# Optimization experiments

Hardware: AMD Instinct MI355X
Metric: run time of the kernel (lower is better)

The kernel has to match this reference:

```python
import jax, jax.numpy as jnp
import numpy as np

ROUTING_ITERS = 3
EPS = 1e-12


def squash(s):
    # squash over both pose-matrix dims (axis=[-2,-1])
    n2 = jnp.sum(s * s, axis=(-2, -1), keepdims=True)
    n = jnp.sqrt(n2 + EPS)
    return s * (n2 / (1.0 + n2)) / n


def setup_inputs() -> dict:
    key = jax.random.key(0)
    k1, k2, k3 = jax.random.split(key, 3)
    B, I, O = 32, 4096, 32
    input_poses = jax.random.normal(k1, (B, I, 4, 4), dtype=jnp.float32)
    input_activations = jax.random.uniform(k2, (B, I), dtype=jnp.float32)
    # weight: [num_capsules, num_input_caps, 4, 4] (trans_in=trans_out=False for 4x4->4x4)
    w = jax.random.normal(k3, (O, I, 4, 4), dtype=jnp.float32) * 0.05
    return {"input_poses": input_poses, "input_activations": input_activations, "w": w}


def reference(input_poses, input_activations, w):
    # votes: expand_dims(poses,1) @ w, broadcast over output capsules -> [B,O,I,4,4]
    votes = jnp.einsum("bixy,oiyz->boixz", input_poses, w)
    B, O, I = votes.shape[0], votes.shape[1], votes.shape[2]

    # dynamic routing (routing-by-agreement)
    b = jnp.zeros((B, O, I), dtype=votes.dtype)
    s = None
    for it in range(ROUTING_ITERS):
        c = jax.nn.softmax(b, axis=1)  # couple over output capsules
        s = jnp.einsum("boi,boixy->boxy", c, votes)  # weighted sum [B,O,4,4]
        if it < ROUTING_ITERS - 1:
            v = squash(s)
            b = b + jnp.einsum("boixy,boxy->boi", votes, v)

    capsule_poses = squash(s)  # activation == 'squash'
    capsule_activations = jnp.sqrt(jnp.sum(capsule_poses * capsule_poses, axis=(-2, -1)) + EPS)
    return capsule_poses, capsule_activations
```

## Files before the change

kernel.cpp:

```cpp
#include <hip/hip_runtime.h>
#include <math.h>


#define NB 32
#define NI 4096
#define NO 32
#define I_TILE 16
#define NCHUNK (NI / I_TILE)
#define B_TILE 8
#define NBG (NB / B_TILE)
#define SOFF (NB * NO * 16)
#define EPSF 1e-12f

#define W_OSTR 10
#define W_ISTR (32 * W_OSTR)
#define W_WORDS (I_TILE * W_ISTR)
#define P_WORDS (B_TILE * I_TILE * 8)

typedef _Float16 v2h __attribute__((ext_vector_type(2)));

#if __has_builtin(__builtin_amdgcn_fdot2)
__device__ __forceinline__ float fdot2(v2h a, v2h b, float c) {
    return __builtin_amdgcn_fdot2(a, b, c, false);
}
#else
__device__ __forceinline__ float fdot2(v2h a, v2h b, float c) {
    return fmaf((float)a.x, (float)b.x, fmaf((float)a.y, (float)b.y, c));
}
#endif

#if __has_builtin(__builtin_amdgcn_cvt_pkrtz)
__device__ __forceinline__ v2h pk2h(float a, float b) {
    return __builtin_bit_cast(v2h, __builtin_amdgcn_cvt_pkrtz(a, b));
}
#else
__device__ __forceinline__ v2h pk2h(float a, float b) {
    v2h r; r.x = (_Float16)a; r.y = (_Float16)b; return r;
}
#endif

__device__ __forceinline__ v2h bch(unsigned u) {
    return __builtin_bit_cast(v2h, u);
}

__device__ __forceinline__ float dot4(const float4 a, const float4 b) {
    return fmaf(a.x, b.x, fmaf(a.y, b.y, fmaf(a.z, b.z, a.w * b.w)));
}

__device__ __forceinline__ void fma4(float4& s, const float c, const float4 t) {
    s.x = fmaf(c, t.x, s.x);
    s.y = fmaf(c, t.y, s.y);
    s.z = fmaf(c, t.z, s.z);
    s.w = fmaf(c, t.w, s.w);
}

template <int CTRL>
__device__ __forceinline__ float dpp_add(float x) {
    int xi = __builtin_bit_cast(int, x);
    int yi = __builtin_amdgcn_update_dpp(0, xi, CTRL, 0xf, 0xf, false);
    return x + __builtin_bit_cast(float, yi);
}

__device__ __forceinline__ float sum32(float x) {
    x = dpp_add<0xB1>(x);
    x = dpp_add<0x4E>(x);
    x = dpp_add<0x141>(x);
    x = dpp_add<0x140>(x);
#if __has_builtin(__builtin_amdgcn_permlane16_swap)
    typedef unsigned uv2 __attribute__((ext_vector_type(2)));
    const unsigned xi = __builtin_bit_cast(unsigned, x);
    uv2 r = __builtin_amdgcn_permlane16_swap(xi, xi, false, false);
    return __builtin_bit_cast(float, r.x) + __builtin_bit_cast(float, r.y);
#else
    int t = __builtin_amdgcn_ds_swizzle(__builtin_bit_cast(int, x), 0x401F);
    return x + __builtin_bit_cast(float, t);
#endif
}

__global__ __launch_bounds__(256, 4) void caps_pass_h(
    const float* __restrict__ poses, const float* __restrict__ w,
    const float* __restrict__ v_buf, float* __restrict__ s_part,
    const int pass)
{
    __shared__ unsigned wsw[W_WORDS];
    __shared__ unsigned psw[P_WORDS];
    const int tid    = threadIdx.x;
    const int chunk  = blockIdx.x;
    const int bgroup = blockIdx.y;
    const int ibase  = chunk * I_TILE;

    #pragma unroll
    for (int r = 0; r < 4; ++r) {
        const int idx = r * 256 + tid;
        const int o_l = idx >> 5;
        const int l   = idx & 31;
        const int i_l = l >> 1;
        const int m   = l & 1;
        const float* g = w + (((size_t)o_l * NI + ibase + i_l) << 4) + (m << 3);
        const float4 A = *(const float4*)g;
        const float4 B = *(const float4*)(g + 4);
        const v2h c0 = pk2h(A.x, B.x), c1 = pk2h(A.y, B.y);
        const v2h c2 = pk2h(A.z, B.z), c3 = pk2h(A.w, B.w);
        const int base = i_l * W_ISTR + o_l * W_OSTR + (m << 2);
        *(uint2*)&wsw[base]     = make_uint2(__builtin_bit_cast(unsigned, c0),
                                             __builtin_bit_cast(unsigned, c1));
        *(uint2*)&wsw[base + 2] = make_uint2(__builtin_bit_cast(unsigned, c2),
                                             __builtin_bit_cast(unsigned, c3));
    }
    #pragma unroll
    for (int r = 0; r < 2; ++r) {
        const int idx = r * 256 + tid;
        const int b_l = idx >> 6;
        const int l   = idx & 63;
        const int i_l = l >> 2;
        const int x   = l & 3;
        const float4 row = *(const float4*)(
            poses + (((size_t)(bgroup * B_TILE + b_l) * NI + ibase + i_l) << 4)
                  + (x << 2));
        const v2h c0 = pk2h(row.x, row.y), c1 = pk2h(row.z, row.w);
        *(uint2*)&psw[((b_l * I_TILE + i_l) << 3) + (x << 1)] =
            make_uint2(__builtin_bit_cast(unsigned, c0),
                       __builtin_bit_cast(unsigned, c1));
    }

    const int o    = tid & 31;
    const int bsub = tid >> 5;
    const int b    = bgroup * B_TILE + bsub;
    const int bo   = b * NO + o;

    float4 vv0 = {0,0,0,0}, vv1 = {0,0,0,0}, vv2 = {0,0,0,0}, vv3 = {0,0,0,0};
    if (pass > 0) {
        const float4* vp = (const float4*)(v_buf + (bo << 4));
        vv0 = vp[0]; vv1 = vp[1]; vv2 = vp[2]; vv3 = vp[3];
    }

    const unsigned* wrow = &wsw[o * W_OSTR];
    const unsigned* prow = &psw[(bsub * I_TILE) << 3];

    __syncthreads();

    float4 s0 = {0,0,0,0}, s1 = {0,0,0,0}, s2 = {0,0,0,0}, s3 = {0,0,0,0};

    #pragma unroll 2
    for (int i = 0; i < I_TILE; ++i) {
        const uint2 wa = *(const uint2*)&wrow[i * W_ISTR + 0];
        const uint2 wb = *(const uint2*)&wrow[i * W_ISTR + 2];
        const uint2 wc = *(const uint2*)&wrow[i * W_ISTR + 4];
        const uint2 wd = *(const uint2*)&wrow[i * W_ISTR + 6];
        const uint4 pa = *(const uint4*)&prow[(i << 3) + 0];
        const uint4 pb = *(const uint4*)&prow[(i << 3) + 4];

        const v2h p00 = bch(pa.x), p01 = bch(pa.y);
        const v2h p10 = bch(pa.z), p11 = bch(pa.w);
        const v2h p20 = bch(pb.x), p21 = bch(pb.y);
        const v2h p30 = bch(pb.z), p31 = bch(pb.w);
        const v2h w00 = bch(wa.x), w01 = bch(wa.y);
        const v2h w02 = bch(wb.x), w03 = bch(wb.y);
        const v2h w10 = bch(wc.x), w11 = bch(wc.y);
        const v2h w12 = bch(wd.x), w13 = bch(wd.y);

        float4 t0, t1, t2, t3;
        t0.x = fdot2(p00, w00, fdot2(p01, w10, 0.0f));
        t0.y = fdot2(p00, w01, fdot2(p01, w11, 0.0f));
        t0.z = fdot2(p00, w02, fdot2(p01, w12, 0.0f));
        t0.w = fdot2(p00, w03, fdot2(p01, w13, 0.0f));
        t1.x = fdot2(p10, w00, fdot2(p11, w10, 0.0f));
        t1.y = fdot2(p10, w01, fdot2(p11, w11, 0.0f));
        t1.z = fdot2(p10, w02, fdot2(p11, w12, 0.0f));
        t1.w = fdot2(p10, w03, fdot2(p11, w13, 0.0f));
        t2.x = fdot2(p20, w00, fdot2(p21, w10, 0.0f));
        t2.y = fdot2(p20, w01, fdot2(p21, w11, 0.0f));
        t2.z = fdot2(p20, w02, fdot2(p21, w12, 0.0f));
        t2.w = fdot2(p20, w03, fdot2(p21, w13, 0.0f));
        t3.x = fdot2(p30, w00, fdot2(p31, w10, 0.0f));
        t3.y = fdot2(p30, w01, fdot2(p31, w11, 0.0f));
        t3.z = fdot2(p30, w02, fdot2(p31, w12, 0.0f));
        t3.w = fdot2(p30, w03, fdot2(p31, w13, 0.0f));

        float cc;
        if (pass == 0) {
            cc = 1.0f / 32.0f;
        } else {
            const float d = dot4(t0,vv0) + dot4(t1,vv1)
                          + dot4(t2,vv2) + dot4(t3,vv3);
            const float e  = __expf(d);
            const float es = sum32(e);
            cc = __fdividef(e, es);
        }
        fma4(s0, cc, t0); fma4(s1, cc, t1);
        fma4(s2, cc, t2); fma4(s3, cc, t3);
    }

    float4* sp = (float4*)(s_part + ((size_t)chunk * (NB * NO) + bo) * 16);
    sp[0] = s0; sp[1] = s1; sp[2] = s2; sp[3] = s3;
}

__global__ __launch_bounds__(256) void caps_reduce(
    const float* __restrict__ s_part, float* __restrict__ v_buf,
    float* __restrict__ out, const int pass)
{
    const int e  = threadIdx.x & 63;
    const int c4 = threadIdx.x >> 6;
    const int eg = blockIdx.x * 64 + e;

    float acc = 0.0f;
    #pragma unroll 8
    for (int j = 0; j < NCHUNK / 4; ++j) {
        const int c = c4 * (NCHUNK / 4) + j;
        acc += s_part[(size_t)c * SOFF + eg];
    }
    __shared__ float red[4][64];
    red[c4][e] = acc;
    __syncthreads();

    if (threadIdx.x < 64) {
        const float a = red[0][e] + red[1][e] + red[2][e] + red[3][e];
        float x = a * a;
        #pragma unroll
        for (int msk = 8; msk >= 1; msk >>= 1)
            x += __shfl_xor(x, msk, 16);
        const float n2 = x;
        const float n  = sqrtf(n2 + EPSF);
        const float sc = (n2 / (1.0f + n2)) / n;
        if (pass < 2) {
            const float vold = (pass == 0) ? 0.0f : v_buf[eg];
            v_buf[eg] = fmaf(sc, a, vold);
        } else {
            out[eg] = sc * a;
            if ((e & 15) == 0)
                out[NB * NO * 16 + (eg >> 4)] = sqrtf(n2 * sc * sc + EPSF);
        }
    }
}

#define FB_CHUNKS 32
#define FB_IPB (NI / FB_CHUNKS)

__device__ __forceinline__ float4 row_mm(const float4 p, const float4 w0,
                                         const float4 w1, const float4 w2,
                                         const float4 w3) {
    float4 r;
    r.x = fmaf(p.x, w0.x, fmaf(p.y, w1.x, fmaf(p.z, w2.x, p.w * w3.x)));
    r.y = fmaf(p.x, w0.y, fmaf(p.y, w1.y, fmaf(p.z, w2.y, p.w * w3.y)));
    r.z = fmaf(p.x, w0.z, fmaf(p.y, w1.z, fmaf(p.z, w2.z, p.w * w3.z)));
    r.w = fmaf(p.x, w0.w, fmaf(p.y, w1.w, fmaf(p.z, w2.w, p.w * w3.w)));
    return r;
}

__global__ __launch_bounds__(256) void caps_pass_fb(
    const float* __restrict__ poses, const float* __restrict__ w,
    const float* __restrict__ v_buf, float* __restrict__ s_buf, const int mode)
{
    const int tid   = threadIdx.x;
    const int b     = blockIdx.y;
    const int chunk = blockIdx.x;
    const int o     = tid & 31;
    const int g     = tid >> 5;

    float4 v0 = {0,0,0,0}, v1 = {0,0,0,0}, v2 = {0,0,0,0}, v3 = {0,0,0,0};
    if (mode != 0) {
        const float4* vp = (const float4*)(v_buf + (((b * NO) + o) << 4));
        v0 = vp[0]; v1 = vp[1]; v2 = vp[2]; v3 = vp[3];
    }
    float4 s0 = {0,0,0,0}, s1 = {0,0,0,0}, s2 = {0,0,0,0}, s3 = {0,0,0,0};
    const int ibase = chunk * FB_IPB + g;
    #pragma unroll 4
    for (int it = 0; it < FB_IPB / 8; ++it) {
        const int i = ibase + (it << 3);
        const float4* ppf = (const float4*)(poses + ((((size_t)b * NI) + i) << 4));
        const float4 p0 = ppf[0], p1 = ppf[1], p2 = ppf[2], p3 = ppf[3];
        const float4* wpf = (const float4*)(w + ((((size_t)o * NI) + i) << 4));
        const float4 w0 = wpf[0], w1 = wpf[1], w2 = wpf[2], w3 = wpf[3];
        const float4 t0 = row_mm(p0, w0, w1, w2, w3);
        const float4 t1 = row_mm(p1, w0, w1, w2, w3);
        const float4 t2 = row_mm(p2, w0, w1, w2, w3);
        const float4 t3 = row_mm(p3, w0, w1, w2, w3);
        float cc;
        if (mode == 0) {
            cc = 1.0f / 32.0f;
        } else {
            float d = dot4(t0,v0) + dot4(t1,v1) + dot4(t2,v2) + dot4(t3,v3);
            const float e  = __expf(d);
            const float es = sum32(e);
            cc = __fdividef(e, es);
        }
        fma4(s0, cc, t0); fma4(s1, cc, t1);
        fma4(s2, cc, t2); fma4(s3, cc, t3);
    }
    __shared__ float red[8][32][16];
    float4* rp = (float4*)&red[g][o][0];
    rp[0] = s0; rp[1] = s1; rp[2] = s2; rp[3] = s3;
    __syncthreads();
    for (int idx = tid; idx < NO * 16; idx += 256) {
        const int oo = idx >> 4;
        const int k  = idx & 15;
        float acc = red[0][oo][k];
        #pragma unroll
        for (int gg = 1; gg < 8; ++gg) acc += red[gg][oo][k];
        atomicAdd(&s_buf[(((b * NO) + oo) << 4) + k], acc);
    }
}

__global__ __launch_bounds__(256) void caps_squash_fb(
    float* __restrict__ s_buf, float* __restrict__ v_buf,
    float* __restrict__ out, const int mode)
{
    const int idx = blockIdx.x * 256 + threadIdx.x;
    if (idx >= NB * NO) return;
    float4* sp = (float4*)(s_buf + (idx << 4));
    const float4 s0 = sp[0], s1 = sp[1], s2 = sp[2], s3 = sp[3];
    const float n2 = dot4(s0,s0) + dot4(s1,s1) + dot4(s2,s2) + dot4(s3,s3);
    const float n  = sqrtf(n2 + EPSF);
    const float sc = (n2 / (1.0f + n2)) / n;
    if (mode == 2) {
        float4* op = (float4*)(out + (idx << 4));
        op[0] = make_float4(sc*s0.x, sc*s0.y, sc*s0.z, sc*s0.w);
        op[1] = make_float4(sc*s1.x, sc*s1.y, sc*s1.z, sc*s1.w);
        op[2] = make_float4(sc*s2.x, sc*s2.y, sc*s2.z, sc*s2.w);
        op[3] = make_float4(sc*s3.x, sc*s3.y, sc*s3.z, sc*s3.w);
        out[NB * NO * 16 + idx] = sqrtf(n2 * sc * sc + EPSF);
    } else {
        float4* vp = (float4*)(v_buf + (idx << 4));
        float4 a0 = {0,0,0,0}, a1 = {0,0,0,0}, a2 = {0,0,0,0}, a3 = {0,0,0,0};
        if (mode != 0) { a0 = vp[0]; a1 = vp[1]; a2 = vp[2]; a3 = vp[3]; }
        vp[0] = make_float4(fmaf(sc,s0.x,a0.x), fmaf(sc,s0.y,a0.y), fmaf(sc,s0.z,a0.z), fmaf(sc,s0.w,a0.w));
        vp[1] = make_float4(fmaf(sc,s1.x,a1.x), fmaf(sc,s1.y,a1.y), fmaf(sc,s1.z,a1.z), fmaf(sc,s1.w,a1.w));
        vp[2] = make_float4(fmaf(sc,s2.x,a2.x), fmaf(sc,s2.y,a2.y), fmaf(sc,s2.z,a2.z), fmaf(sc,s2.w,a2.w));
        vp[3] = make_float4(fmaf(sc,s3.x,a3.x), fmaf(sc,s3.y,a3.y), fmaf(sc,s3.z,a3.z), fmaf(sc,s3.w,a3.w));
        const float4 z = {0,0,0,0};
        sp[0] = z; sp[1] = z; sp[2] = z; sp[3] = z;
    }
}

extern "C" void kernel_launch(void* const* d_in, const int* in_sizes, int n_in,
                              void* d_out, int out_size, void* d_ws, size_t ws_size,
                              hipStream_t stream) {
    const float* poses = (const float*)d_in[0];
    const float* w     = (const float*)d_in[2];
    float* out = (float*)d_out;

    const size_t need = ((size_t)NCHUNK * SOFF + SOFF) * sizeof(float);
    if (ws_size >= need) {
        float* s_part = (float*)d_ws;
        float* v_buf  = s_part + (size_t)NCHUNK * SOFF;
        dim3 gp(NCHUNK, NBG), blk(256), gr(256);
        for (int pass = 0; pass < 3; ++pass) {
            caps_pass_h<<<gp, blk, 0, stream>>>(poses, w, v_buf, s_part, pass);
            caps_reduce<<<gr, blk, 0, stream>>>(s_part, v_buf, out, pass);
        }
    } else {
        float* s_buf = (float*)d_ws;
        float* v_buf = s_buf + SOFF;
        (void)hipMemsetAsync(s_buf, 0, SOFF * sizeof(float), stream);
        dim3 grid(FB_CHUNKS, NB), block(256);
        for (int pass = 0; pass < 3; ++pass) {
            caps_pass_fb<<<grid, block, 0, stream>>>(poses, w, v_buf, s_buf, pass);
            caps_squash_fb<<<4, 256, 0, stream>>>(s_buf, v_buf, out, pass);
        }
    }
}
```

Baseline: 130.5 us.

## Use 1024-thread blocks covering all batches so weight tiles load once per chunk

The pass kernel now runs one 1024-thread block per input chunk that covers all 32 batch rows, instead of four 256-thread blocks that each covered 8 rows. Each weight tile is therefore read from global memory and converted to half once per chunk rather than four times. Pose loads become wider 8-float loads stored as uint4, and the partial-sum output layout is changed to float4-interleaved columns, with the reduce kernel's indexing updated to match. This costs fewer blocks (256), larger per-block LDS, and possible occupancy limits under launch_bounds(1024,4). The cvt_pkrtz conversion builtin is also replaced with plain half casts.

```diff
diff --git a/kernel.cpp b/kernel.cpp
--- a/kernel.cpp
+++ b/kernel.cpp
@@ -7,15 +7,13 @@
 #define NO 32
 #define I_TILE 16
 #define NCHUNK (NI / I_TILE)
-#define B_TILE 8
-#define NBG (NB / B_TILE)
 #define SOFF (NB * NO * 16)
 #define EPSF 1e-12f
 
 #define W_OSTR 10
 #define W_ISTR (32 * W_OSTR)
 #define W_WORDS (I_TILE * W_ISTR)
-#define P_WORDS (B_TILE * I_TILE * 8)
+#define P_WORDS (NB * I_TILE * 8)
 
 typedef _Float16 v2h __attribute__((ext_vector_type(2)));
 
@@ -29,15 +27,13 @@
 }
 #endif
 
-#if __has_builtin(__builtin_amdgcn_cvt_pkrtz)
-__device__ __forceinline__ v2h pk2h(float a, float b) {
-    return __builtin_bit_cast(v2h, __builtin_amdgcn_cvt_pkrtz(a, b));
-}
-#else
 __device__ __forceinline__ v2h pk2h(float a, float b) {
     v2h r; r.x = (_Float16)a; r.y = (_Float16)b; return r;
 }
-#endif
+
+__device__ __forceinline__ unsigned ubits(v2h x) {
+    return __builtin_bit_cast(unsigned, x);
+}
 
 __device__ __forceinline__ v2h bch(unsigned u) {
     return __builtin_bit_cast(v2h, u);
@@ -77,56 +73,49 @@
 #endif
 }
 
-__global__ __launch_bounds__(256, 4) void caps_pass_h(
+__global__ __launch_bounds__(1024, 4) void caps_pass_w(
     const float* __restrict__ poses, const float* __restrict__ w,
     const float* __restrict__ v_buf, float* __restrict__ s_part,
     const int pass)
 {
     __shared__ unsigned wsw[W_WORDS];
     __shared__ unsigned psw[P_WORDS];
-    const int tid    = threadIdx.x;
-    const int chunk  = blockIdx.x;
-    const int bgroup = blockIdx.y;
-    const int ibase  = chunk * I_TILE;
-
-    #pragma unroll
-    for (int r = 0; r < 4; ++r) {
-        const int idx = r * 256 + tid;
-        const int o_l = idx >> 5;
-        const int l   = idx & 31;
-        const int i_l = l >> 1;
-        const int m   = l & 1;
+    const int tid   = threadIdx.x;
+    const int chunk = blockIdx.x;
+    const int ibase = chunk * I_TILE;
+
+    {
+        const int o_l = tid >> 5;
+        const int rem = tid & 31;
+        const int i_l = rem >> 1;
+        const int m   = rem & 1;
         const float* g = w + (((size_t)o_l * NI + ibase + i_l) << 4) + (m << 3);
         const float4 A = *(const float4*)g;
         const float4 B = *(const float4*)(g + 4);
-        const v2h c0 = pk2h(A.x, B.x), c1 = pk2h(A.y, B.y);
-        const v2h c2 = pk2h(A.z, B.z), c3 = pk2h(A.w, B.w);
         const int base = i_l * W_ISTR + o_l * W_OSTR + (m << 2);
-        *(uint2*)&wsw[base]     = make_uint2(__builtin_bit_cast(unsigned, c0),
-                                             __builtin_bit_cast(unsigned, c1));
-        *(uint2*)&wsw[base + 2] = make_uint2(__builtin_bit_cast(unsigned, c2),
-                                             __builtin_bit_cast(unsigned, c3));
-    }
-    #pragma unroll
-    for (int r = 0; r < 2; ++r) {
-        const int idx = r * 256 + tid;
-        const int b_l = idx >> 6;
-        const int l   = idx & 63;
-        const int i_l = l >> 2;
-        const int x   = l & 3;
-        const float4 row = *(const float4*)(
-            poses + (((size_t)(bgroup * B_TILE + b_l) * NI + ibase + i_l) << 4)
-                  + (x << 2));
-        const v2h c0 = pk2h(row.x, row.y), c1 = pk2h(row.z, row.w);
-        *(uint2*)&psw[((b_l * I_TILE + i_l) << 3) + (x << 1)] =
-            make_uint2(__builtin_bit_cast(unsigned, c0),
-                       __builtin_bit_cast(unsigned, c1));
+        *(uint2*)&wsw[base]     = make_uint2(ubits(pk2h(A.x, B.x)),
+                                             ubits(pk2h(A.y, B.y)));
+        *(uint2*)&wsw[base + 2] = make_uint2(ubits(pk2h(A.z, B.z)),
+                                             ubits(pk2h(A.w, B.w)));
+    }
+    {
+        const int b_l = tid >> 5;
+        const int rem = tid & 31;
+        const int i_l = rem >> 1;
+        const int x2  = rem & 1;
+        const float* g = poses + (((size_t)b_l * NI + ibase + i_l) << 4)
+                       + (x2 << 3);
+        const float4 A = *(const float4*)g;
+        const float4 B = *(const float4*)(g + 4);
+        uint4 st;
+        st.x = ubits(pk2h(A.x, A.y)); st.y = ubits(pk2h(A.z, A.w));
+        st.z = ubits(pk2h(B.x, B.y)); st.w = ubits(pk2h(B.z, B.w));
+        *(uint4*)&psw[((b_l * I_TILE + i_l) << 3) + (x2 << 2)] = st;
     }
 
     const int o    = tid & 31;
     const int bsub = tid >> 5;
-    const int b    = bgroup * B_TILE + bsub;
-    const int bo   = b * NO + o;
+    const int bo   = bsub * NO + o;
 
     float4 vv0 = {0,0,0,0}, vv1 = {0,0,0,0}, vv2 = {0,0,0,0}, vv3 = {0,0,0,0};
     if (pass > 0) {
@@ -191,8 +180,11 @@
         fma4(s2, cc, t2); fma4(s3, cc, t3);
     }
 
-    float4* sp = (float4*)(s_part + ((size_t)chunk * (NB * NO) + bo) * 16);
-    sp[0] = s0; sp[1] = s1; sp[2] = s2; sp[3] = s3;
+    float4* sp = (float4*)s_part;
+    sp[(size_t)((chunk << 2) + 0) * (NB * NO) + bo] = s0;
+    sp[(size_t)((chunk << 2) + 1) * (NB * NO) + bo] = s1;
+    sp[(size_t)((chunk << 2) + 2) * (NB * NO) + bo] = s2;
+    sp[(size_t)((chunk << 2) + 3) * (NB * NO) + bo] = s3;
 }
 
 __global__ __launch_bounds__(256) void caps_reduce(
@@ -202,12 +194,15 @@
     const int e  = threadIdx.x & 63;
     const int c4 = threadIdx.x >> 6;
     const int eg = blockIdx.x * 64 + e;
+    const int bo   = eg >> 4;
+    const int k    = eg & 15;
+    const int col  = ((k >> 2) << 12) + (bo << 2) + (k & 3);
 
     float acc = 0.0f;
     #pragma unroll 8
     for (int j = 0; j < NCHUNK / 4; ++j) {
         const int c = c4 * (NCHUNK / 4) + j;
-        acc += s_part[(size_t)c * SOFF + eg];
+        acc += s_part[(size_t)c * SOFF + col];
     }
     __shared__ float red[4][64];
     red[c4][e] = acc;
@@ -227,8 +222,8 @@
             v_buf[eg] = fmaf(sc, a, vold);
         } else {
             out[eg] = sc * a;
-            if ((e & 15) == 0)
-                out[NB * NO * 16 + (eg >> 4)] = sqrtf(n2 * sc * sc + EPSF);
+            if (k == 0)
+                out[NB * NO * 16 + bo] = sqrtf(n2 * sc * sc + EPSF);
         }
     }
 }
@@ -293,11 +288,11 @@
     __syncthreads();
     for (int idx = tid; idx < NO * 16; idx += 256) {
         const int oo = idx >> 4;
-        const int k  = idx & 15;
-        float acc = red[0][oo][k];
+        const int kk = idx & 15;
+        float acc = red[0][oo][kk];
         #pragma unroll
-        for (int gg = 1; gg < 8; ++gg) acc += red[gg][oo][k];
-        atomicAdd(&s_buf[(((b * NO) + oo) << 4) + k], acc);
+        for (int gg = 1; gg < 8; ++gg) acc += red[gg][oo][kk];
+        atomicAdd(&s_buf[(((b * NO) + oo) << 4) + kk], acc);
     }
 }
 
@@ -343,10 +338,10 @@
     if (ws_size >= need) {
         float* s_part = (float*)d_ws;
         float* v_buf  = s_part + (size_t)NCHUNK * SOFF;
-        dim3 gp(NCHUNK, NBG), blk(256), gr(256);
+        dim3 gp(NCHUNK), blkp(1024), gr(256), blkr(256);
         for (int pass = 0; pass < 3; ++pass) {
-            caps_pass_h<<<gp, blk, 0, stream>>>(poses, w, v_buf, s_part, pass);
-            caps_reduce<<<gr, blk, 0, stream>>>(s_part, v_buf, out, pass);
+            caps_pass_w<<<gp, blkp, 0, stream>>>(poses, w, v_buf, s_part, pass);
+            caps_reduce<<<gr, blkr, 0, stream>>>(s_part, v_buf, out, pass);
         }
     } else {
         float* s_buf = (float*)d_ws;
```

New measurement: 136.7 us. 4.8% more time.
